# Kernel optimization log

Hardware: AMD Instinct MI355X
Metric: run time of the kernel (lower is better)

## Reference

```python
import jax, jax.numpy as jnp
import numpy as np

N_NODES = 100000


def spmm(edge_src, edge_dst, edge_val, x):
    """z[dst] += val * x[src] over all edges (COO sparse-dense matmul)."""
    gathered = edge_val[:, None] * x[edge_src]  # [E, d]
    return jax.ops.segment_sum(gathered, edge_dst, num_segments=N_NODES)


def setup_inputs() -> dict:
    key = jax.random.key(0)
    k1, k2, k3, k4, k5, k6 = jax.random.split(key, 6)
    N, E, IN, H, C = N_NODES, 1600000, 256, 128, 40
    features = jax.random.normal(k1, (N, IN), dtype=jnp.float32)
    # xavier_uniform-like init
    b1 = float(np.sqrt(6.0 / (IN + H)))
    b2 = float(np.sqrt(6.0 / (H + C)))
    W1 = jax.random.uniform(k2, (IN, H), dtype=jnp.float32, minval=-b1, maxval=b1)
    W2 = jax.random.uniform(k3, (H, C), dtype=jnp.float32, minval=-b2, maxval=b2)
    edge_src = jax.random.randint(k4, (E,), 0, N, dtype=jnp.int32)
    edge_dst = jnp.sort(jax.random.randint(k5, (E,), 0, N, dtype=jnp.int32))
    # normalized-adjacency-like positive edge weights
    edge_val = jax.random.uniform(k6, (E,), dtype=jnp.float32)
    return {"features": features, "W1": W1, "W2": W2,
            "edge_src": edge_src, "edge_dst": edge_dst, "edge_val": edge_val}


def reference(features, W1, W2, edge_src, edge_dst, edge_val):
    # Decoupled GCN: all dense NN layers first (relu between, none after last) ...
    h = jax.nn.relu(features @ W1)
    h = h @ W2  # [N, num_classes]
    # ... then nlayers (=2) rounds of graph propagation (spmm aggregation)
    h = spmm(edge_src, edge_dst, edge_val, h)
    h = spmm(edge_src, edge_dst, edge_val, h)
    return h
```

## Files before the change

### kernel.cpp

```cpp
#include <hip/hip_runtime.h>
#include <cstddef>
#include <cstdint>

#define IN_DIM 256
#define H_DIM  128
#define C_DIM  40
#define BM     128
#define LDQ    68
#define PAD_C  40
#define STEP   512

typedef short bf16x8 __attribute__((ext_vector_type(8)));
typedef float f32x16 __attribute__((ext_vector_type(16)));
typedef uint  u32x4  __attribute__((ext_vector_type(4)));

__device__ __forceinline__ ushort f2bf(float f) {
  uint u = __builtin_bit_cast(uint, f);
  u += 0x7fffu + ((u >> 16) & 1u);
  return (ushort)(u >> 16);
}
__device__ __forceinline__ float bf2f(uint s) {
  uint u = s << 16;
  return __builtin_bit_cast(float, u);
}
__device__ __forceinline__ uint pack2bf(float a, float b) {
#if __has_builtin(__builtin_amdgcn_cvt_pk_bf16_f32)
  typedef __bf16 bf16v2 __attribute__((ext_vector_type(2)));
  bf16v2 r = __builtin_amdgcn_cvt_pk_bf16_f32(a, b);
  return __builtin_bit_cast(uint, r);
#else
  return (uint)f2bf(a) | ((uint)f2bf(b) << 16);
#endif
}

__global__ void setup_kernel(const int* __restrict__ dst, int E,
                             int* __restrict__ row_ptr, int N,
                             const float* __restrict__ W1,
                             const float* __restrict__ W2,
                             ushort* __restrict__ b_frag,
                             ushort* __restrict__ w2f) {
  int tid = blockIdx.x * blockDim.x + threadIdx.x;
  if (tid < E) {
    int d1 = dst[tid];
    int d0 = (tid == 0) ? -1 : dst[tid - 1];
    for (int v = d0 + 1; v <= d1; ++v) row_ptr[v] = tid;
    if (tid == E - 1)
      for (int v = d1 + 1; v <= N; ++v) row_ptr[v] = E;
    return;
  }
  int u = tid - E;
  if (u < 4096) {
    int l = u & 63, ks = (u >> 6) & 15, tn = u >> 10;
    int n  = 32 * tn + (l & 31);
    int k0 = ks * 16 + ((l >> 5) << 3);
    ushort r[8];
#pragma unroll
    for (int j = 0; j < 8; ++j) r[j] = f2bf(W1[(k0 + j) * H_DIM + n]);
    *(uint4*)(b_frag + u * 8) = *(uint4*)r;
    return;
  }
  u -= 4096;
  if (u < 1024) {
    int l = u & 63, kt = u >> 6;
    int tn = kt & 1, kb = kt >> 1;
    int n  = 32 * tn + (l & 31);
    int k0 = kb * 16 + ((l >> 5) << 3);
    ushort r[8];
#pragma unroll
    for (int j = 0; j < 8; ++j)
      r[j] = (n < C_DIM) ? f2bf(W2[(k0 + j) * C_DIM + n]) : (ushort)0;
    *(uint4*)(w2f + u * 8) = *(uint4*)r;
  }
}

__global__ __launch_bounds__(256, 4) void fused_dense_kernel(
    const float* __restrict__ feat, const ushort* __restrict__ b_frag,
    const ushort* __restrict__ w2f, ushort* __restrict__ z0, int N) {
  __shared__ __align__(16) ushort smem[4 * 32 * LDQ];

  const int t = threadIdx.x;
  const int w = t >> 6, l = t & 63;
  const int nb = blockIdx.x * BM;
  ushort* slab = smem + w * (32 * LDQ);

  const int sr = l >> 4;
  const int sc = l & 15;

  f32x16 acc[4];
#pragma unroll
  for (int tn = 0; tn < 4; ++tn)
#pragma unroll
    for (int r = 0; r < 16; ++r) acc[tn][r] = 0.f;

  const ushort* bp = b_frag + l * 8;
  bf16x8 Bx[2][4];
#pragma unroll
  for (int tn = 0; tn < 4; ++tn)
    Bx[0][tn] = *(const bf16x8*)(bp + tn * (16 * STEP));

  const float* fbase = feat + (size_t)(nb + 32 * w) * IN_DIM + sc * 4;

  float4 pre[8];
#pragma unroll
  for (int c = 0; c < 8; ++c) {
    int grow = nb + 32 * w + 4 * c + sr;
    const float* p = fbase + (size_t)(4 * c + sr) * IN_DIM;
    if (grow >= N) p = feat + (size_t)(N - 1) * IN_DIM + sc * 4;
    pre[c] = *(const float4*)(p);
  }
#pragma unroll
  for (int c = 0; c < 8; ++c) {
    uint2 pk;
    pk.x = pack2bf(pre[c].x, pre[c].y);
    pk.y = pack2bf(pre[c].z, pre[c].w);
    *(uint2*)(slab + (4 * c + sr) * LDQ + sc * 4) = pk;
  }

  const ushort* Abase = slab + (l & 31) * LDQ + ((l >> 5) << 3);

#pragma unroll
  for (int q = 0; q < 4; ++q) {
#pragma unroll
    for (int ks = 0; ks < 4; ++ks) {
      const int gks = 4 * q + ks;
      const int c = gks & 1;
      if (gks < 15) {
#pragma unroll
        for (int tn = 0; tn < 4; ++tn)
          Bx[c ^ 1][tn] = *(const bf16x8*)(bp + tn * (16 * STEP) + (gks + 1) * STEP);
      }
      if (q < 3) {
#pragma unroll
        for (int d = 0; d < 2; ++d) {
          const int cc = 2 * ks + d;
          int grow = nb + 32 * w + 4 * cc + sr;
          const float* p = fbase + (size_t)(4 * cc + sr) * IN_DIM + (q + 1) * 64;
          if (grow >= N) p = feat + (size_t)(N - 1) * IN_DIM + sc * 4 + (q + 1) * 64;
          pre[cc] = *(const float4*)(p);
        }
      }
      bf16x8 af = *(const bf16x8*)(Abase + ks * 16);
#pragma unroll
      for (int tn = 0; tn < 4; ++tn)
        acc[tn] = __builtin_amdgcn_mfma_f32_32x32x16_bf16(af, Bx[c][tn], acc[tn], 0, 0, 0);
    }
    if (q < 3) {
#pragma unroll
      for (int c = 0; c < 8; ++c) {
        uint2 pk;
        pk.x = pack2bf(pre[c].x, pre[c].y);
        pk.y = pack2bf(pre[c].z, pre[c].w);
        *(uint2*)(slab + (4 * c + sr) * LDQ + sc * 4) = pk;
      }
    }
  }

  f32x16 acc2[2];
#pragma unroll
  for (int tn = 0; tn < 2; ++tn)
#pragma unroll
    for (int r = 0; r < 16; ++r) acc2[tn][r] = 0.f;

  const ushort* Hbase = slab + (l & 31) * LDQ + ((l >> 5) << 3);
  const ushort* wp = w2f + l * 8;

#pragma unroll
  for (int hc = 0; hc < 2; ++hc) {
#pragma unroll
    for (int tn = 2 * hc; tn < 2 * hc + 2; ++tn) {
      int col = (tn - 2 * hc) * 32 + (l & 31);
#pragma unroll
      for (int r = 0; r < 16; ++r) {
        int nl = (r & 3) + 8 * (r >> 2) + 4 * (l >> 5);
        float v = acc[tn][r];
        slab[nl * LDQ + col] = f2bf(v > 0.f ? v : 0.f);
      }
    }
#pragma unroll
    for (int kb = 4 * hc; kb < 4 * hc + 4; ++kb) {
      bf16x8 af = *(const bf16x8*)(Hbase + (kb - 4 * hc) * 16);
#pragma unroll
      for (int tn = 0; tn < 2; ++tn) {
        bf16x8 bfr = *(const bf16x8*)(wp + (kb * 2 + tn) * STEP);
        acc2[tn] = __builtin_amdgcn_mfma_f32_32x32x16_bf16(af, bfr, acc2[tn], 0, 0, 0);
      }
    }
  }

#pragma unroll
  for (int tn = 0; tn < 2; ++tn) {
    int col = tn * 32 + (l & 31);
    if (col < C_DIM) {
#pragma unroll
      for (int r = 0; r < 16; ++r) {
        int node = nb + 32 * w + (r & 3) + 8 * (r >> 2) + 4 * (l >> 5);
        if (node < N) z0[(size_t)node * PAD_C + col] = f2bf(acc2[tn][r]);
      }
    }
  }
}

__global__ __launch_bounds__(256) void spmm_kernel(
    const int* __restrict__ row_ptr, const int* __restrict__ esrc,
    const float* __restrict__ eval, const ushort* __restrict__ x,
    ushort* __restrict__ zb, float* __restrict__ zf, int N, int out_f32) {
  int node = (blockIdx.x << 2) + (threadIdx.x >> 6);
  if (node >= N) return;
  const int lane = threadIdx.x & 63;
  const int h = lane >> 3;
  const int j = lane & 7;
  const bool act = (j < 5);

  int e   = row_ptr[node];
  int end = row_ptr[node + 1];

  float acc[8];
#pragma unroll
  for (int c = 0; c < 8; ++c) acc[c] = 0.f;

  for (; e + 16 <= end; e += 16) {
    int   s0 = esrc[e + h];
    int   s1 = esrc[e + 8 + h];
    float v0 = eval[e + h];
    float v1 = eval[e + 8 + h];
    if (act) {
      u32x4 a = *(const u32x4*)(x + (size_t)s0 * PAD_C + j * 8);
      u32x4 b = *(const u32x4*)(x + (size_t)s1 * PAD_C + j * 8);
      acc[0] = fmaf(v0, bf2f(a.x & 0xffffu), acc[0]);
      acc[1] = fmaf(v0, bf2f(a.x >> 16),     acc[1]);
      acc[2] = fmaf(v0, bf2f(a.y & 0xffffu), acc[2]);
      acc[3] = fmaf(v0, bf2f(a.y >> 16),     acc[3]);
      acc[4] = fmaf(v0, bf2f(a.z & 0xffffu), acc[4]);
      acc[5] = fmaf(v0, bf2f(a.z >> 16),     acc[5]);
      acc[6] = fmaf(v0, bf2f(a.w & 0xffffu), acc[6]);
      acc[7] = fmaf(v0, bf2f(a.w >> 16),     acc[7]);
      acc[0] = fmaf(v1, bf2f(b.x & 0xffffu), acc[0]);
      acc[1] = fmaf(v1, bf2f(b.x >> 16),     acc[1]);
      acc[2] = fmaf(v1, bf2f(b.y & 0xffffu), acc[2]);
      acc[3] = fmaf(v1, bf2f(b.y >> 16),     acc[3]);
      acc[4] = fmaf(v1, bf2f(b.z & 0xffffu), acc[4]);
      acc[5] = fmaf(v1, bf2f(b.z >> 16),     acc[5]);
      acc[6] = fmaf(v1, bf2f(b.w & 0xffffu), acc[6]);
      acc[7] = fmaf(v1, bf2f(b.w >> 16),     acc[7]);
    }
  }
  for (; e + 8 <= end; e += 8) {
    int   s = esrc[e + h];
    float v = eval[e + h];
    if (act) {
      u32x4 u = *(const u32x4*)(x + (size_t)s * PAD_C + j * 8);
      acc[0] = fmaf(v, bf2f(u.x & 0xffffu), acc[0]);
      acc[1] = fmaf(v, bf2f(u.x >> 16),     acc[1]);
      acc[2] = fmaf(v, bf2f(u.y & 0xffffu), acc[2]);
      acc[3] = fmaf(v, bf2f(u.y >> 16),     acc[3]);
      acc[4] = fmaf(v, bf2f(u.z & 0xffffu), acc[4]);
      acc[5] = fmaf(v, bf2f(u.z >> 16),     acc[5]);
      acc[6] = fmaf(v, bf2f(u.w & 0xffffu), acc[6]);
      acc[7] = fmaf(v, bf2f(u.w >> 16),     acc[7]);
    }
  }
  if (e < end) {
    int ei = e + h;
    int ec = ei < end ? ei : end - 1;
    int   s  = esrc[ec];
    float v0 = eval[ec];
    float v  = ei < end ? v0 : 0.f;
    if (act) {
      u32x4 u = *(const u32x4*)(x + (size_t)s * PAD_C + j * 8);
      acc[0] = fmaf(v, bf2f(u.x & 0xffffu), acc[0]);
      acc[1] = fmaf(v, bf2f(u.x >> 16),     acc[1]);
      acc[2] = fmaf(v, bf2f(u.y & 0xffffu), acc[2]);
      acc[3] = fmaf(v, bf2f(u.y >> 16),     acc[3]);
      acc[4] = fmaf(v, bf2f(u.z & 0xffffu), acc[4]);
      acc[5] = fmaf(v, bf2f(u.z >> 16),     acc[5]);
      acc[6] = fmaf(v, bf2f(u.w & 0xffffu), acc[6]);
      acc[7] = fmaf(v, bf2f(u.w >> 16),     acc[7]);
    }
  }

#pragma unroll
  for (int c = 0; c < 8; ++c) acc[c] += __shfl_xor(acc[c], 8);
#pragma unroll
  for (int c = 0; c < 8; ++c) acc[c] += __shfl_xor(acc[c], 16);
#pragma unroll
  for (int c = 0; c < 8; ++c) acc[c] += __shfl_xor(acc[c], 32);

  if (out_f32) {
    if (lane < 5) {
      float4 o0 = {acc[0], acc[1], acc[2], acc[3]};
      float4 o1 = {acc[4], acc[5], acc[6], acc[7]};
      float* p = zf + (size_t)node * C_DIM + j * 8;
      *(float4*)(p + 0) = o0;
      *(float4*)(p + 4) = o1;
    }
  } else {
    if (lane < 5) {
      uint4 p;
      p.x = (uint)f2bf(acc[0]) | ((uint)f2bf(acc[1]) << 16);
      p.y = (uint)f2bf(acc[2]) | ((uint)f2bf(acc[3]) << 16);
      p.z = (uint)f2bf(acc[4]) | ((uint)f2bf(acc[5]) << 16);
      p.w = (uint)f2bf(acc[6]) | ((uint)f2bf(acc[7]) << 16);
      *(uint4*)(zb + (size_t)node * PAD_C + j * 8) = p;
    }
  }
}

extern "C" void kernel_launch(void* const* d_in, const int* in_sizes, int n_in,
                              void* d_out, int out_size, void* d_ws, size_t ws_size,
                              hipStream_t stream) {
  const float* feat  = (const float*)d_in[0];
  const float* W1    = (const float*)d_in[1];
  const float* W2    = (const float*)d_in[2];
  const int*   esrc  = (const int*)d_in[3];
  const int*   edst  = (const int*)d_in[4];
  const float* evalp = (const float*)d_in[5];
  float* out = (float*)d_out;

  const int N = in_sizes[0] / IN_DIM;
  const int E = in_sizes[3];

  const int nblk = (N + BM - 1) / BM;

  char* ws = (char*)d_ws;
  ushort* z0     = (ushort*)ws;
  ushort* z1     = (ushort*)(ws + (size_t)N * PAD_C * 2);
  ushort* b_frag = (ushort*)(ws + (size_t)N * PAD_C * 4);
  ushort* w2f    = b_frag + 4 * 16 * STEP;
  int* row_ptr   = (int*)(w2f + 16 * STEP);

  const int setup_items = E + 4096 + 1024;
  setup_kernel<<<(setup_items + 255) / 256, 256, 0, stream>>>(
      edst, E, row_ptr, N, W1, W2, b_frag, w2f);
  fused_dense_kernel<<<nblk, 256, 0, stream>>>(feat, b_frag, w2f, z0, N);
  spmm_kernel<<<(N + 3) / 4, 256, 0, stream>>>(row_ptr, esrc, evalp, z0, z1, nullptr, N, 0);
  spmm_kernel<<<(N + 3) / 4, 256, 0, stream>>>(row_ptr, esrc, evalp, z1, nullptr, out, N, 1);
}
```

Measured before the change: 272.9 us.

## Split 40-wide bf16 node features into 32+8 arrays for denser SpMM gathers

Stores the intermediate features as two arrays: a 32-column bf16 array (64B rows) and an 8-column bf16 array (16B rows). The SpMM kernel now uses 4 lanes per edge on the main array, so 16 edges are processed per wavefront step instead of 8 with 3 of 8 lanes idle. Lane 0 of each group also gathers the extra 8 columns. This aims to raise lane utilisation and align gathers to cache lines, at the cost of a second gather per edge into a separate array and divergent single-lane work.

```diff
diff --git a/kernel.cpp b/kernel.cpp
--- a/kernel.cpp
+++ b/kernel.cpp
@@ -7,7 +7,8 @@
 #define C_DIM  40
 #define BM     128
 #define LDQ    68
-#define PAD_C  40
+#define XA_C   32
+#define XB_C   8
 #define STEP   512
 
 typedef short bf16x8 __attribute__((ext_vector_type(8)));
@@ -75,7 +76,8 @@
 
 __global__ __launch_bounds__(256, 4) void fused_dense_kernel(
     const float* __restrict__ feat, const ushort* __restrict__ b_frag,
-    const ushort* __restrict__ w2f, ushort* __restrict__ z0, int N) {
+    const ushort* __restrict__ w2f, ushort* __restrict__ z0a,
+    ushort* __restrict__ z0b, int N) {
   __shared__ __align__(16) ushort smem[4 * 32 * LDQ];
 
   const int t = threadIdx.x;
@@ -188,75 +190,100 @@
   }
 
 #pragma unroll
-  for (int tn = 0; tn < 2; ++tn) {
-    int col = tn * 32 + (l & 31);
-    if (col < C_DIM) {
-#pragma unroll
-      for (int r = 0; r < 16; ++r) {
-        int node = nb + 32 * w + (r & 3) + 8 * (r >> 2) + 4 * (l >> 5);
-        if (node < N) z0[(size_t)node * PAD_C + col] = f2bf(acc2[tn][r]);
-      }
+  for (int r = 0; r < 16; ++r) {
+    int node = nb + 32 * w + (r & 3) + 8 * (r >> 2) + 4 * (l >> 5);
+    if (node < N) {
+      z0a[(size_t)node * XA_C + (l & 31)] = f2bf(acc2[0][r]);
+      if ((l & 31) < XB_C)
+        z0b[(size_t)node * XB_C + (l & 31)] = f2bf(acc2[1][r]);
     }
   }
 }
 
 __global__ __launch_bounds__(256) void spmm_kernel(
     const int* __restrict__ row_ptr, const int* __restrict__ esrc,
-    const float* __restrict__ eval, const ushort* __restrict__ x,
-    ushort* __restrict__ zb, float* __restrict__ zf, int N, int out_f32) {
+    const float* __restrict__ eval, const ushort* __restrict__ xa,
+    const ushort* __restrict__ xb, ushort* __restrict__ za,
+    ushort* __restrict__ zb8, float* __restrict__ zf, int N, int out_f32) {
   int node = (blockIdx.x << 2) + (threadIdx.x >> 6);
   if (node >= N) return;
   const int lane = threadIdx.x & 63;
-  const int h = lane >> 3;
-  const int j = lane & 7;
-  const bool act = (j < 5);
+  const int h = lane >> 2;
+  const int j = lane & 3;
 
   int e   = row_ptr[node];
   int end = row_ptr[node + 1];
 
-  float acc[8];
-#pragma unroll
-  for (int c = 0; c < 8; ++c) acc[c] = 0.f;
-
+  float acc[8], accb[8];
+#pragma unroll
+  for (int c = 0; c < 8; ++c) { acc[c] = 0.f; accb[c] = 0.f; }
+
+  for (; e + 32 <= end; e += 32) {
+    int   s0 = esrc[e + h];
+    int   s1 = esrc[e + 16 + h];
+    float v0 = eval[e + h];
+    float v1 = eval[e + 16 + h];
+    u32x4 a = *(const u32x4*)(xa + (size_t)s0 * XA_C + j * 8);
+    u32x4 b = *(const u32x4*)(xa + (size_t)s1 * XA_C + j * 8);
+    acc[0] = fmaf(v0, bf2f(a.x & 0xffffu), acc[0]);
+    acc[1] = fmaf(v0, bf2f(a.x >> 16),     acc[1]);
+    acc[2] = fmaf(v0, bf2f(a.y & 0xffffu), acc[2]);
+    acc[3] = fmaf(v0, bf2f(a.y >> 16),     acc[3]);
+    acc[4] = fmaf(v0, bf2f(a.z & 0xffffu), acc[4]);
+    acc[5] = fmaf(v0, bf2f(a.z >> 16),     acc[5]);
+    acc[6] = fmaf(v0, bf2f(a.w & 0xffffu), acc[6]);
+    acc[7] = fmaf(v0, bf2f(a.w >> 16),     acc[7]);
+    acc[0] = fmaf(v1, bf2f(b.x & 0xffffu), acc[0]);
+    acc[1] = fmaf(v1, bf2f(b.x >> 16),     acc[1]);
+    acc[2] = fmaf(v1, bf2f(b.y & 0xffffu), acc[2]);
+    acc[3] = fmaf(v1, bf2f(b.y >> 16),     acc[3]);
+    acc[4] = fmaf(v1, bf2f(b.z & 0xffffu), acc[4]);
+    acc[5] = fmaf(v1, bf2f(b.z >> 16),     acc[5]);
+    acc[6] = fmaf(v1, bf2f(b.w & 0xffffu), acc[6]);
+    acc[7] = fmaf(v1, bf2f(b.w >> 16),     acc[7]);
+    if (j == 0) {
+      u32x4 p = *(const u32x4*)(xb + (size_t)s0 * XB_C);
+      u32x4 q = *(const u32x4*)(xb + (size_t)s1 * XB_C);
+      accb[0] = fmaf(v0, bf2f(p.x & 0xffffu), accb[0]);
+      accb[1] = fmaf(v0, bf2f(p.x >> 16),     accb[1]);
+      accb[2] = fmaf(v0, bf2f(p.y & 0xffffu), accb[2]);
+      accb[3] = fmaf(v0, bf2f(p.y >> 16),     accb[3]);
+      accb[4] = fmaf(v0, bf2f(p.z & 0xffffu), accb[4]);
+      accb[5] = fmaf(v0, bf2f(p.z >> 16),     accb[5]);
+      accb[6] = fmaf(v0, bf2f(p.w & 0xffffu), accb[6]);
+      accb[7] = fmaf(v0, bf2f(p.w >> 16),     accb[7]);
+      accb[0] = fmaf(v1, bf2f(q.x & 0xffffu), accb[0]);
+      accb[1] = fmaf(v1, bf2f(q.x >> 16),     accb[1]);
+      accb[2] = fmaf(v1, bf2f(q.y & 0xffffu), accb[2]);
+      accb[3] = fmaf(v1, bf2f(q.y >> 16),     accb[3]);
+      accb[4] = fmaf(v1, bf2f(q.z & 0xffffu), accb[4]);
+      accb[5] = fmaf(v1, bf2f(q.z >> 16),     accb[5]);
+      accb[6] = fmaf(v1, bf2f(q.w & 0xffffu), accb[6]);
+      accb[7] = fmaf(v1, bf2f(q.w >> 16),     accb[7]);
+    }
+  }
   for (; e + 16 <= end; e += 16) {
-    int   s0 = esrc[e + h];
-    int   s1 = esrc[e + 8 + h];
-    float v0 = eval[e + h];
-    float v1 = eval[e + 8 + h];
-    if (act) {
-      u32x4 a = *(const u32x4*)(x + (size_t)s0 * PAD_C + j * 8);
-      u32x4 b = *(const u32x4*)(x + (size_t)s1 * PAD_C + j * 8);
-      acc[0] = fmaf(v0, bf2f(a.x & 0xffffu), acc[0]);
-      acc[1] = fmaf(v0, bf2f(a.x >> 16),     acc[1]);
-      acc[2] = fmaf(v0, bf2f(a.y & 0xffffu), acc[2]);
-      acc[3] = fmaf(v0, bf2f(a.y >> 16),     acc[3]);
-      acc[4] = fmaf(v0, bf2f(a.z & 0xffffu), acc[4]);
-      acc[5] = fmaf(v0, bf2f(a.z >> 16),     acc[5]);
-      acc[6] = fmaf(v0, bf2f(a.w & 0xffffu), acc[6]);
-      acc[7] = fmaf(v0, bf2f(a.w >> 16),     acc[7]);
-      acc[0] = fmaf(v1, bf2f(b.x & 0xffffu), acc[0]);
-      acc[1] = fmaf(v1, bf2f(b.x >> 16),     acc[1]);
-      acc[2] = fmaf(v1, bf2f(b.y & 0xffffu), acc[2]);
-      acc[3] = fmaf(v1, bf2f(b.y >> 16),     acc[3]);
-      acc[4] = fmaf(v1, bf2f(b.z & 0xffffu), acc[4]);
-      acc[5] = fmaf(v1, bf2f(b.z >> 16),     acc[5]);
-      acc[6] = fmaf(v1, bf2f(b.w & 0xffffu), acc[6]);
-      acc[7] = fmaf(v1, bf2f(b.w >> 16),     acc[7]);
-    }
-  }
-  for (; e + 8 <= end; e += 8) {
     int   s = esrc[e + h];
     float v = eval[e + h];
-    if (act) {
-      u32x4 u = *(const u32x4*)(x + (size_t)s * PAD_C + j * 8);
-      acc[0] = fmaf(v, bf2f(u.x & 0xffffu), acc[0]);
-      acc[1] = fmaf(v, bf2f(u.x >> 16),     acc[1]);
-      acc[2] = fmaf(v, bf2f(u.y & 0xffffu), acc[2]);
-      acc[3] = fmaf(v, bf2f(u.y >> 16),     acc[3]);
-      acc[4] = fmaf(v, bf2f(u.z & 0xffffu), acc[4]);
-      acc[5] = fmaf(v, bf2f(u.z >> 16),     acc[5]);
-      acc[6] = fmaf(v, bf2f(u.w & 0xffffu), acc[6]);
-      acc[7] = fmaf(v, bf2f(u.w >> 16),     acc[7]);
+    u32x4 a = *(const u32x4*)(xa + (size_t)s * XA_C + j * 8);
+    acc[0] = fmaf(v, bf2f(a.x & 0xffffu), acc[0]);
+    acc[1] = fmaf(v, bf2f(a.x >> 16),     acc[1]);
+    acc[2] = fmaf(v, bf2f(a.y & 0xffffu), acc[2]);
+    acc[3] = fmaf(v, bf2f(a.y >> 16),     acc[3]);
+    acc[4] = fmaf(v, bf2f(a.z & 0xffffu), acc[4]);
+    acc[5] = fmaf(v, bf2f(a.z >> 16),     acc[5]);
+    acc[6] = fmaf(v, bf2f(a.w & 0xffffu), acc[6]);
+    acc[7] = fmaf(v, bf2f(a.w >> 16),     acc[7]);
+    if (j == 0) {
+      u32x4 p = *(const u32x4*)(xb + (size_t)s * XB_C);
+      accb[0] = fmaf(v, bf2f(p.x & 0xffffu), accb[0]);
+      accb[1] = fmaf(v, bf2f(p.x >> 16),     accb[1]);
+      accb[2] = fmaf(v, bf2f(p.y & 0xffffu), accb[2]);
+      accb[3] = fmaf(v, bf2f(p.y >> 16),     accb[3]);
+      accb[4] = fmaf(v, bf2f(p.z & 0xffffu), accb[4]);
+      accb[5] = fmaf(v, bf2f(p.z >> 16),     accb[5]);
+      accb[6] = fmaf(v, bf2f(p.w & 0xffffu), accb[6]);
+      accb[7] = fmaf(v, bf2f(p.w >> 16),     accb[7]);
     }
   }
   if (e < end) {
@@ -265,42 +292,68 @@
     int   s  = esrc[ec];
     float v0 = eval[ec];
     float v  = ei < end ? v0 : 0.f;
-    if (act) {
-      u32x4 u = *(const u32x4*)(x + (size_t)s * PAD_C + j * 8);
-      acc[0] = fmaf(v, bf2f(u.x & 0xffffu), acc[0]);
-      acc[1] = fmaf(v, bf2f(u.x >> 16),     acc[1]);
-      acc[2] = fmaf(v, bf2f(u.y & 0xffffu), acc[2]);
-      acc[3] = fmaf(v, bf2f(u.y >> 16),     acc[3]);
-      acc[4] = fmaf(v, bf2f(u.z & 0xffffu), acc[4]);
-      acc[5] = fmaf(v, bf2f(u.z >> 16),     acc[5]);
-      acc[6] = fmaf(v, bf2f(u.w & 0xffffu), acc[6]);
-      acc[7] = fmaf(v, bf2f(u.w >> 16),     acc[7]);
-    }
-  }
-
-#pragma unroll
-  for (int c = 0; c < 8; ++c) acc[c] += __shfl_xor(acc[c], 8);
-#pragma unroll
-  for (int c = 0; c < 8; ++c) acc[c] += __shfl_xor(acc[c], 16);
-#pragma unroll
-  for (int c = 0; c < 8; ++c) acc[c] += __shfl_xor(acc[c], 32);
+    u32x4 a = *(const u32x4*)(xa + (size_t)s * XA_C + j * 8);
+    acc[0] = fmaf(v, bf2f(a.x & 0xffffu), acc[0]);
+    acc[1] = fmaf(v, bf2f(a.x >> 16),     acc[1]);
+    acc[2] = fmaf(v, bf2f(a.y & 0xffffu), acc[2]);
+    acc[3] = fmaf(v, bf2f(a.y >> 16),     acc[3]);
+    acc[4] = fmaf(v, bf2f(a.z & 0xffffu), acc[4]);
+    acc[5] = fmaf(v, bf2f(a.z >> 16),     acc[5]);
+    acc[6] = fmaf(v, bf2f(a.w & 0xffffu), acc[6]);
+    acc[7] = fmaf(v, bf2f(a.w >> 16),     acc[7]);
+    if (j == 0) {
+      u32x4 p = *(const u32x4*)(xb + (size_t)s * XB_C);
+      accb[0] = fmaf(v, bf2f(p.x & 0xffffu), accb[0]);
+      accb[1] = fmaf(v, bf2f(p.x >> 16),     accb[1]);
+      accb[2] = fmaf(v, bf2f(p.y & 0xffffu), accb[2]);
+      accb[3] = fmaf(v, bf2f(p.y >> 16),     accb[3]);
+      accb[4] = fmaf(v, bf2f(p.z & 0xffffu), accb[4]);
+      accb[5] = fmaf(v, bf2f(p.z >> 16),     accb[5]);
+      accb[6] = fmaf(v, bf2f(p.w & 0xffffu), accb[6]);
+      accb[7] = fmaf(v, bf2f(p.w >> 16),     accb[7]);
+    }
+  }
+
+#pragma unroll
+  for (int c = 0; c < 8; ++c) { acc[c] += __shfl_xor(acc[c], 4);  accb[c] += __shfl_xor(accb[c], 4); }
+#pragma unroll
+  for (int c = 0; c < 8; ++c) { acc[c] += __shfl_xor(acc[c], 8);  accb[c] += __shfl_xor(accb[c], 8); }
+#pragma unroll
+  for (int c = 0; c < 8; ++c) { acc[c] += __shfl_xor(acc[c], 16); accb[c] += __shfl_xor(accb[c], 16); }
+#pragma unroll
+  for (int c = 0; c < 8; ++c) { acc[c] += __shfl_xor(acc[c], 32); accb[c] += __shfl_xor(accb[c], 32); }
 
   if (out_f32) {
-    if (lane < 5) {
+    if (lane < 4) {
       float4 o0 = {acc[0], acc[1], acc[2], acc[3]};
       float4 o1 = {acc[4], acc[5], acc[6], acc[7]};
       float* p = zf + (size_t)node * C_DIM + j * 8;
       *(float4*)(p + 0) = o0;
       *(float4*)(p + 4) = o1;
     }
+    if (lane == 0) {
+      float4 o0 = {accb[0], accb[1], accb[2], accb[3]};
+      float4 o1 = {accb[4], accb[5], accb[6], accb[7]};
+      float* p = zf + (size_t)node * C_DIM + 32;
+      *(float4*)(p + 0) = o0;
+      *(float4*)(p + 4) = o1;
+    }
   } else {
-    if (lane < 5) {
+    if (lane < 4) {
       uint4 p;
       p.x = (uint)f2bf(acc[0]) | ((uint)f2bf(acc[1]) << 16);
       p.y = (uint)f2bf(acc[2]) | ((uint)f2bf(acc[3]) << 16);
       p.z = (uint)f2bf(acc[4]) | ((uint)f2bf(acc[5]) << 16);
       p.w = (uint)f2bf(acc[6]) | ((uint)f2bf(acc[7]) << 16);
-      *(uint4*)(zb + (size_t)node * PAD_C + j * 8) = p;
+      *(uint4*)(za + (size_t)node * XA_C + j * 8) = p;
+    }
+    if (lane == 0) {
+      uint4 p;
+      p.x = (uint)f2bf(accb[0]) | ((uint)f2bf(accb[1]) << 16);
+      p.y = (uint)f2bf(accb[2]) | ((uint)f2bf(accb[3]) << 16);
+      p.z = (uint)f2bf(accb[4]) | ((uint)f2bf(accb[5]) << 16);
+      p.w = (uint)f2bf(accb[6]) | ((uint)f2bf(accb[7]) << 16);
+      *(uint4*)(zb8 + (size_t)node * XB_C) = p;
     }
   }
 }
@@ -322,16 +375,20 @@
   const int nblk = (N + BM - 1) / BM;
 
   char* ws = (char*)d_ws;
-  ushort* z0     = (ushort*)ws;
-  ushort* z1     = (ushort*)(ws + (size_t)N * PAD_C * 2);
-  ushort* b_frag = (ushort*)(ws + (size_t)N * PAD_C * 4);
+  ushort* z0a    = (ushort*)ws;
+  ushort* z0b    = z0a + (size_t)N * XA_C;
+  ushort* z1a    = z0b + (size_t)N * XB_C;
+  ushort* z1b    = z1a + (size_t)N * XA_C;
+  ushort* b_frag = z1b + (size_t)N * XB_C;
   ushort* w2f    = b_frag + 4 * 16 * STEP;
   int* row_ptr   = (int*)(w2f + 16 * STEP);
 
   const int setup_items = E + 4096 + 1024;
   setup_kernel<<<(setup_items + 255) / 256, 256, 0, stream>>>(
       edst, E, row_ptr, N, W1, W2, b_frag, w2f);
-  fused_dense_kernel<<<nblk, 256, 0, stream>>>(feat, b_frag, w2f, z0, N);
-  spmm_kernel<<<(N + 3) / 4, 256, 0, stream>>>(row_ptr, esrc, evalp, z0, z1, nullptr, N, 0);
-  spmm_kernel<<<(N + 3) / 4, 256, 0, stream>>>(row_ptr, esrc, evalp, z1, nullptr, out, N, 1);
-}
+  fused_dense_kernel<<<nblk, 256, 0, stream>>>(feat, b_frag, w2f, z0a, z0b, N);
+  spmm_kernel<<<(N + 3) / 4, 256, 0, stream>>>(row_ptr, esrc, evalp, z0a, z0b,
+                                               z1a, z1b, nullptr, N, 0);
+  spmm_kernel<<<(N + 3) / 4, 256, 0, stream>>>(row_ptr, esrc, evalp, z1a, z1b,
+                                               nullptr, nullptr, out, N, 1);
+}
```

Measured after the change: 330.4 us. +21.1%, slower.
